# Performance work log

Measured on AMD Instinct MI355X. Metric: run time of the kernel, lower is better.

Reference implementation:

```python
import jax, jax.numpy as jnp
import numpy as np

E, H, I = 16, 2048, 768
B, S = 4, 1024
TOPK = 8
BLK_R, BLK_C = 128, 128


def blockwise_dequantize(w, scale_inv, r, c):
    # w: [E, M, N] (fp8 values stored as fp32 here), scale_inv: [E, M//r, N//c]
    e, m, n = w.shape
    wb = w.reshape(e, m // r, r, n // c, c)
    wb = wb * scale_inv[:, :, None, :, None]
    return wb.reshape(e, m, n)


def setup_inputs() -> dict:
    key = jax.random.key(0)
    ks = jax.random.split(key, 7)
    return {
        "hidden_states": jax.random.normal(ks[0], (B, S, H), dtype=jnp.float32),
        "routing_weights": jax.random.uniform(ks[1], (B * S, E), dtype=jnp.float32),
        "gate_up_proj": jax.random.normal(ks[2], (E, H, 2 * I), dtype=jnp.float32),
        "gate_up_proj_scale_inv": jax.random.uniform(ks[3], (E, H // BLK_R, 2 * I // BLK_C), dtype=jnp.float32),
        "down_proj": jax.random.normal(ks[4], (E, I, H), dtype=jnp.float32),
        "down_proj_scale_inv": jax.random.uniform(ks[5], (E, I // BLK_R, H // BLK_C), dtype=jnp.float32),
        "router_indices": jax.random.randint(ks[6], (B * S, TOPK), 0, E, dtype=jnp.int64 if jax.config.jax_enable_x64 else jnp.int32),
    }


def reference(hidden_states, routing_weights, gate_up_proj, gate_up_proj_scale_inv,
              down_proj, down_proj_scale_inv, router_indices):
    batch_size = hidden_states.shape[0]
    hs = hidden_states.reshape(-1, H)                      # [T, H], T = B*S
    x = jnp.broadcast_to(hs[None], (E,) + hs.shape)        # repeat across experts

    gu_w = blockwise_dequantize(gate_up_proj, gate_up_proj_scale_inv, BLK_R, BLK_C)   # [E, H, 2I]
    dn_w = blockwise_dequantize(down_proj, down_proj_scale_inv, BLK_R, BLK_C)         # [E, I, H]

    gate_up = jnp.einsum('eth,ehf->etf', x, gu_w)          # [E, T, 2I]
    gate, up = jnp.split(gate_up, 2, axis=-1)
    inter = up * jax.nn.silu(gate)                         # [E, T, I]
    next_states = jnp.einsum('eti,eih->eth', inter, dn_w)  # [E, T, H]

    next_states = next_states.reshape(E, batch_size, -1, H)
    rw = routing_weights.T.reshape(E, batch_size, -1)      # [E, B, S]
    out = (next_states * rw[..., None]).sum(axis=0)        # [B, S, H]
    return out
```

## Files before the change

kernel.cpp:

```cpp
#include <hip/hip_runtime.h>
#include <hip/hip_bf16.h>
#include <cstdint>

#define E_     16
#define H_     2048
#define I_     768
#define T_     4096
#define TWO_I  1536
#define K2_    (E_ * I_)
#define TILE_  (128 * 32)

typedef __bf16 bf16x8 __attribute__((ext_vector_type(8)));
typedef float  floatx4 __attribute__((ext_vector_type(4)));

__device__ __forceinline__ void gload_lds16(const void* g, void* l) {
  __builtin_amdgcn_global_load_lds(
      (const __attribute__((address_space(1))) void*)(void*)g,
      (__attribute__((address_space(3))) void*)l,
      16, 0, 0);
}

__global__ void k_convert(const float* __restrict__ in, __bf16* __restrict__ out) {
  size_t idx = ((size_t)blockIdx.x * blockDim.x + threadIdx.x) * 8;
  float4 a = *(const float4*)(in + idx);
  float4 b = *(const float4*)(in + idx + 4);
  bf16x8 o;
  o[0] = (__bf16)a.x; o[1] = (__bf16)a.y; o[2] = (__bf16)a.z; o[3] = (__bf16)a.w;
  o[4] = (__bf16)b.x; o[5] = (__bf16)b.y; o[6] = (__bf16)b.z; o[7] = (__bf16)b.w;
  *(bf16x8*)(out + idx) = o;
}

__global__ void k_dq_transpose(const float* __restrict__ src, __bf16* __restrict__ dst,
                               const float* __restrict__ scale, int R, int C,
                               size_t slab, size_t rowStride) {
  const int e  = blockIdx.z;
  const int n0 = blockIdx.x * 64;
  const int m0 = blockIdx.y * 64;
  __shared__ float tile[64 * 65];
  const float s = scale[((size_t)e * (R >> 7) + (m0 >> 7)) * (C >> 7) + (n0 >> 7)];
  const float* sp = src + ((size_t)e * R + m0) * C + n0;
  const int t  = threadIdx.x;
  const int c4 = (t & 15) * 4;
  const int rb = t >> 4;
  #pragma unroll
  for (int p = 0; p < 4; ++p) {
    int r = p * 16 + rb;
    float4 v = *(const float4*)(sp + (size_t)r * C + c4);
    tile[(c4 + 0) * 65 + r] = v.x * s;
    tile[(c4 + 1) * 65 + r] = v.y * s;
    tile[(c4 + 2) * 65 + r] = v.z * s;
    tile[(c4 + 3) * 65 + r] = v.w * s;
  }
  __syncthreads();
  __bf16* dp = dst + (size_t)e * slab + (size_t)n0 * rowStride + m0;
  const int c8 = (t & 7) * 8;
  const int r0 = t >> 3;
  #pragma unroll
  for (int p = 0; p < 2; ++p) {
    int nr = r0 + p * 32;
    const float* row = &tile[nr * 65 + c8];
    bf16x8 o;
    #pragma unroll
    for (int j = 0; j < 8; ++j) o[j] = (__bf16)row[j];
    *(bf16x8*)(dp + (size_t)nr * rowStride + c8) = o;
  }
}

__global__ __launch_bounds__(256, 2)
void k_gemm1(const __bf16* __restrict__ A, const __bf16* __restrict__ W,
             const float* __restrict__ rw, __bf16* __restrict__ inter) {
  const int e  = blockIdx.z;
  const int m0 = blockIdx.x * 128;
  const int i0 = blockIdx.y * 128;
  __shared__ __bf16 sA[2 * TILE_];
  __shared__ __bf16 sBg[2 * TILE_];
  __shared__ __bf16 sBu[2 * TILE_];
  __shared__ float sRW[128];
  const int t = threadIdx.x;
  const int wave = t >> 6, lane = t & 63;
  if (t < 128) sRW[t] = rw[(size_t)(m0 + t) * E_ + e];

  const int srow = lane >> 2;
  const int scol = (lane & 3) * 8;
  const int wm = wave >> 1, wn = wave & 1;
  const int r16 = lane & 15, kh = (lane >> 4) * 8;

  const size_t off0 = (size_t)(wave * 16 + srow) * H_ + scol;
  const size_t off1 = (size_t)((4 + wave) * 16 + srow) * H_ + scol;
  const __bf16* pa = A + (size_t)m0 * H_;
  const __bf16* pg = W + ((size_t)e * TWO_I + i0) * H_;
  const __bf16* pu = pg + (size_t)I_ * H_;
  __bf16* lA0 = &sA[(wave * 16) * 32];
  __bf16* lA1 = &sA[((4 + wave) * 16) * 32];
  __bf16* lG0 = &sBg[(wave * 16) * 32];
  __bf16* lG1 = &sBg[((4 + wave) * 16) * 32];
  __bf16* lU0 = &sBu[(wave * 16) * 32];
  __bf16* lU1 = &sBu[((4 + wave) * 16) * 32];

  floatx4 accg[4][4], accu[4][4];
  #pragma unroll
  for (int mi = 0; mi < 4; ++mi)
    #pragma unroll
    for (int ni = 0; ni < 4; ++ni) {
      floatx4 z = {0.f, 0.f, 0.f, 0.f};
      accg[mi][ni] = z; accu[mi][ni] = z;
    }

  for (int k0 = 0; k0 < H_; k0 += 64) {
    #pragma unroll
    for (int h = 0; h < 2; ++h) {
      const int kb = k0 + h * 32;
      const int ho = h * TILE_;
      gload_lds16(pa + off0 + kb, lA0 + ho);
      gload_lds16(pa + off1 + kb, lA1 + ho);
      gload_lds16(pg + off0 + kb, lG0 + ho);
      gload_lds16(pg + off1 + kb, lG1 + ho);
      gload_lds16(pu + off0 + kb, lU0 + ho);
      gload_lds16(pu + off1 + kb, lU1 + ho);
    }
    __syncthreads();
    #pragma unroll
    for (int h = 0; h < 2; ++h) {
      const int ho = h * TILE_;
      bf16x8 af[4], bg[4], bu[4];
      #pragma unroll
      for (int mi = 0; mi < 4; ++mi)
        af[mi] = *(const bf16x8*)&sA[ho + (wm * 64 + mi * 16 + r16) * 32 + kh];
      #pragma unroll
      for (int ni = 0; ni < 4; ++ni) {
        bg[ni] = *(const bf16x8*)&sBg[ho + (wn * 64 + ni * 16 + r16) * 32 + kh];
        bu[ni] = *(const bf16x8*)&sBu[ho + (wn * 64 + ni * 16 + r16) * 32 + kh];
      }
      #pragma unroll
      for (int mi = 0; mi < 4; ++mi)
        #pragma unroll
        for (int ni = 0; ni < 4; ++ni) {
          accg[mi][ni] = __builtin_amdgcn_mfma_f32_16x16x32_bf16(af[mi], bg[ni], accg[mi][ni], 0, 0, 0);
          accu[mi][ni] = __builtin_amdgcn_mfma_f32_16x16x32_bf16(af[mi], bu[ni], accu[mi][ni], 0, 0, 0);
        }
    }
    __syncthreads();
  }

  const int rq = (lane >> 4) * 4;
  #pragma unroll
  for (int mi = 0; mi < 4; ++mi) {
    #pragma unroll
    for (int ni = 0; ni < 4; ++ni) {
      const int cl = wn * 64 + ni * 16 + r16;
      #pragma unroll
      for (int r = 0; r < 4; ++r) {
        const int rl = wm * 64 + mi * 16 + rq + r;
        float g = accg[mi][ni][r];
        float u = accu[mi][ni][r];
        float sil = g / (1.0f + __expf(-g));
        float val = u * sil * sRW[rl];
        inter[(size_t)(m0 + rl) * K2_ + (size_t)e * I_ + i0 + cl] = (__bf16)val;
      }
    }
  }
}

__global__ __launch_bounds__(256, 2)
void k_gemm2(const __bf16* __restrict__ Ainter, const __bf16* __restrict__ W,
             float* __restrict__ out) {
  const int m0 = blockIdx.x * 128;
  const int n0 = blockIdx.y * 128;
  __shared__ __bf16 sA[2 * TILE_];
  __shared__ __bf16 sB[2 * TILE_];
  const int t = threadIdx.x;
  const int wave = t >> 6, lane = t & 63;
  const int srow = lane >> 2, scol = (lane & 3) * 8;
  const int wm = wave >> 1, wn = wave & 1;
  const int r16 = lane & 15, kh = (lane >> 4) * 8;

  const size_t off0 = (size_t)(wave * 16 + srow) * K2_ + scol;
  const size_t off1 = (size_t)((4 + wave) * 16 + srow) * K2_ + scol;
  const __bf16* pa = Ainter + (size_t)m0 * K2_;
  const __bf16* pb = W + (size_t)n0 * K2_;
  __bf16* lA0 = &sA[(wave * 16) * 32];
  __bf16* lA1 = &sA[((4 + wave) * 16) * 32];
  __bf16* lB0 = &sB[(wave * 16) * 32];
  __bf16* lB1 = &sB[((4 + wave) * 16) * 32];

  floatx4 acc[4][4];
  #pragma unroll
  for (int mi = 0; mi < 4; ++mi)
    #pragma unroll
    for (int ni = 0; ni < 4; ++ni) {
      floatx4 z = {0.f, 0.f, 0.f, 0.f};
      acc[mi][ni] = z;
    }

  for (int k0 = 0; k0 < K2_; k0 += 64) {
    #pragma unroll
    for (int h = 0; h < 2; ++h) {
      const int kb = k0 + h * 32;
      const int ho = h * TILE_;
      gload_lds16(pa + off0 + kb, lA0 + ho);
      gload_lds16(pa + off1 + kb, lA1 + ho);
      gload_lds16(pb + off0 + kb, lB0 + ho);
      gload_lds16(pb + off1 + kb, lB1 + ho);
    }
    __syncthreads();
    #pragma unroll
    for (int h = 0; h < 2; ++h) {
      const int ho = h * TILE_;
      bf16x8 af[4], bb[4];
      #pragma unroll
      for (int mi = 0; mi < 4; ++mi)
        af[mi] = *(const bf16x8*)&sA[ho + (wm * 64 + mi * 16 + r16) * 32 + kh];
      #pragma unroll
      for (int ni = 0; ni < 4; ++ni)
        bb[ni] = *(const bf16x8*)&sB[ho + (wn * 64 + ni * 16 + r16) * 32 + kh];
      #pragma unroll
      for (int mi = 0; mi < 4; ++mi)
        #pragma unroll
        for (int ni = 0; ni < 4; ++ni)
          acc[mi][ni] = __builtin_amdgcn_mfma_f32_16x16x32_bf16(af[mi], bb[ni], acc[mi][ni], 0, 0, 0);
    }
    __syncthreads();
  }

  const int rq = (lane >> 4) * 4;
  #pragma unroll
  for (int mi = 0; mi < 4; ++mi)
    #pragma unroll
    for (int ni = 0; ni < 4; ++ni) {
      const int cl = wn * 64 + ni * 16 + r16;
      #pragma unroll
      for (int r = 0; r < 4; ++r) {
        const int rl = wm * 64 + mi * 16 + rq + r;
        out[(size_t)(m0 + rl) * H_ + n0 + cl] = acc[mi][ni][r];
      }
    }
}

extern "C" void kernel_launch(void* const* d_in, const int* in_sizes, int n_in,
                              void* d_out, int out_size, void* d_ws, size_t ws_size,
                              hipStream_t stream) {
  const float* hs   = (const float*)d_in[0];
  const float* rw   = (const float*)d_in[1];
  const float* gup  = (const float*)d_in[2];
  const float* gups = (const float*)d_in[3];
  const float* dnp  = (const float*)d_in[4];
  const float* dnps = (const float*)d_in[5];
  float* out = (float*)d_out;

  char* ws = (char*)d_ws;
  __bf16* hsb  = (__bf16*)ws;
  __bf16* wgu  = (__bf16*)(ws + (size_t)(16 << 20));
  __bf16* wdn  = (__bf16*)(ws + (size_t)(112 << 20));
  __bf16* intr = (__bf16*)(ws + (size_t)(160 << 20));

  k_convert<<<(T_ * H_) / (256 * 8), 256, 0, stream>>>(hs, hsb);
  k_dq_transpose<<<dim3(TWO_I / 64, H_ / 64, E_), 256, 0, stream>>>(
      gup, wgu, gups, H_, TWO_I, (size_t)TWO_I * H_, (size_t)H_);
  k_dq_transpose<<<dim3(H_ / 64, I_ / 64, E_), 256, 0, stream>>>(
      dnp, wdn, dnps, I_, H_, (size_t)I_, (size_t)K2_);
  k_gemm1<<<dim3(T_ / 128, I_ / 128, E_), 256, 0, stream>>>(hsb, wgu, rw, intr);
  k_gemm2<<<dim3(T_ / 128, H_ / 128), 256, 0, stream>>>(intr, wdn, out);
}
```

Measured before the change: 1.078 ms.

## Rewrite MoE GEMMs with 256x256 tiles, swizzled LDS, pipelined staging and split-K

Both GEMMs move to 512-thread blocks computing 256x256 tiles, with XOR-swizzled LDS layouts and a double-buffered, phase-interleaved prefetch schedule built from explicit waitcnt, barriers and setprio. The gate and up weights are interleaved in 32-column groups by the dequant-transpose kernel, so a single B tile holds matching gate and up columns. The down projection is split over K into two halves that accumulate into a zeroed output with atomic adds. This aims to raise MFMA utilization and data reuse per LDS load, at the cost of about 128KB of dynamic LDS per block, atomic traffic and an extra memset.

```diff
diff --git a/kernel.cpp b/kernel.cpp
--- a/kernel.cpp
+++ b/kernel.cpp
@@ -8,7 +8,6 @@
 #define T_     4096
 #define TWO_I  1536
 #define K2_    (E_ * I_)
-#define TILE_  (128 * 32)
 
 typedef __bf16 bf16x8 __attribute__((ext_vector_type(8)));
 typedef float  floatx4 __attribute__((ext_vector_type(4)));
@@ -19,6 +18,11 @@
       (__attribute__((address_space(3))) void*)l,
       16, 0, 0);
 }
+
+#define ASM_VMCNT(n) asm volatile("s_waitcnt vmcnt(" #n ")" ::: "memory")
+#define ASM_LGKM0()  asm volatile("s_waitcnt lgkmcnt(0)" ::: "memory")
+#define SBAR()       __builtin_amdgcn_s_barrier()
+#define SCHED0()     __builtin_amdgcn_sched_barrier(0)
 
 __global__ void k_convert(const float* __restrict__ in, __bf16* __restrict__ out) {
   size_t idx = ((size_t)blockIdx.x * blockDim.x + threadIdx.x) * 8;
@@ -32,7 +36,7 @@
 
 __global__ void k_dq_transpose(const float* __restrict__ src, __bf16* __restrict__ dst,
                                const float* __restrict__ scale, int R, int C,
-                               size_t slab, size_t rowStride) {
+                               size_t slab, size_t rowStride, int ilvHalf) {
   const int e  = blockIdx.z;
   const int n0 = blockIdx.x * 64;
   const int m0 = blockIdx.y * 64;
@@ -52,188 +56,222 @@
     tile[(c4 + 3) * 65 + r] = v.w * s;
   }
   __syncthreads();
-  __bf16* dp = dst + (size_t)e * slab + (size_t)n0 * rowStride + m0;
   const int c8 = (t & 7) * 8;
   const int r0 = t >> 3;
   #pragma unroll
   for (int p = 0; p < 2; ++p) {
     int nr = r0 + p * 32;
+    int ng = n0 + nr;
+    int np;
+    if (ilvHalf) {
+      int h = (ng >= ilvHalf) ? 1 : 0;
+      int iLoc = ng - h * ilvHalf;
+      np = ((iLoc >> 5) << 6) + h * 32 + (iLoc & 31);
+    } else {
+      np = ng;
+    }
     const float* row = &tile[nr * 65 + c8];
     bf16x8 o;
     #pragma unroll
     for (int j = 0; j < 8; ++j) o[j] = (__bf16)row[j];
-    *(bf16x8*)(dp + (size_t)nr * rowStride + c8) = o;
-  }
-}
-
-__global__ __launch_bounds__(256, 2)
+    *(bf16x8*)(dst + (size_t)e * slab + (size_t)np * rowStride + m0 + c8) = o;
+  }
+}
+
+
+#define STG_A(tt, h) do { int b_ = ((tt)&1)*16384 + (h)*8192; \
+    gload_lds16(aSrc + (size_t)((h)*128)*LDK + (tt)*64, dA + b_); \
+    gload_lds16(aSrc + (size_t)((h)*128 + 64)*LDK + (tt)*64, dA + b_ + 4096); } while (0)
+#define STG_B(tt, h) do { int b_ = ((tt)&1)*16384 + (h)*8192; \
+    gload_lds16(bSrc + (size_t)((h)*128)*LDK + (tt)*64, dB + b_); \
+    gload_lds16(bSrc + (size_t)((h)*128 + 64)*LDK + (tt)*64, dB + b_ + 4096); } while (0)
+
+#define AF4(MI0) do { \
+    af[0][0] = *(const bf16x8*)(pA + (MI0)*1024 + kc0); \
+    af[0][1] = *(const bf16x8*)(pA + (MI0)*1024 + kc1); \
+    af[1][0] = *(const bf16x8*)(pA + ((MI0)+1)*1024 + kc0); \
+    af[1][1] = *(const bf16x8*)(pA + ((MI0)+1)*1024 + kc1); } while (0)
+
+#define MFMA16(MI0) do { \
+    _Pragma("unroll") \
+    for (int ii = 0; ii < 2; ++ii) { \
+      _Pragma("unroll") \
+      for (int ni = 0; ni < 4; ++ni) { \
+        acc[(MI0)+ii][ni] = __builtin_amdgcn_mfma_f32_16x16x32_bf16(af[ii][0], bb[ni][0], acc[(MI0)+ii][ni], 0, 0, 0); \
+        acc[(MI0)+ii][ni] = __builtin_amdgcn_mfma_f32_16x16x32_bf16(af[ii][1], bb[ni][1], acc[(MI0)+ii][ni], 0, 0, 0); \
+      } \
+    } } while (0)
+
+#define PHASE(MI0, STAGE_STMT, CKPT_STMT) do { \
+    AF4(MI0); \
+    STAGE_STMT; \
+    CKPT_STMT; \
+    SBAR(); \
+    ASM_LGKM0(); \
+    SCHED0(); \
+    __builtin_amdgcn_s_setprio(1); \
+    MFMA16(MI0); \
+    __builtin_amdgcn_s_setprio(0); \
+    SBAR(); \
+  } while (0)
+
+__global__ __launch_bounds__(512, 2)
 void k_gemm1(const __bf16* __restrict__ A, const __bf16* __restrict__ W,
              const float* __restrict__ rw, __bf16* __restrict__ inter) {
+  extern __shared__ __align__(16) __bf16 smem[];
+  __bf16* sA = smem;
+  __bf16* sB = smem + 32768;
+  float*  sRW = (float*)(smem + 65536);
+
   const int e  = blockIdx.z;
-  const int m0 = blockIdx.x * 128;
-  const int i0 = blockIdx.y * 128;
-  __shared__ __bf16 sA[2 * TILE_];
-  __shared__ __bf16 sBg[2 * TILE_];
-  __shared__ __bf16 sBu[2 * TILE_];
-  __shared__ float sRW[128];
-  const int t = threadIdx.x;
+  const int m0 = blockIdx.x * 256;
+  const int by = blockIdx.y;
+  const int n0 = by * 256;
+  const int t    = threadIdx.x;
   const int wave = t >> 6, lane = t & 63;
-  if (t < 128) sRW[t] = rw[(size_t)(m0 + t) * E_ + e];
-
-  const int srow = lane >> 2;
-  const int scol = (lane & 3) * 8;
-  const int wm = wave >> 1, wn = wave & 1;
-  const int r16 = lane & 15, kh = (lane >> 4) * 8;
-
-  const size_t off0 = (size_t)(wave * 16 + srow) * H_ + scol;
-  const size_t off1 = (size_t)((4 + wave) * 16 + srow) * H_ + scol;
-  const __bf16* pa = A + (size_t)m0 * H_;
-  const __bf16* pg = W + ((size_t)e * TWO_I + i0) * H_;
-  const __bf16* pu = pg + (size_t)I_ * H_;
-  __bf16* lA0 = &sA[(wave * 16) * 32];
-  __bf16* lA1 = &sA[((4 + wave) * 16) * 32];
-  __bf16* lG0 = &sBg[(wave * 16) * 32];
-  __bf16* lG1 = &sBg[((4 + wave) * 16) * 32];
-  __bf16* lU0 = &sBu[(wave * 16) * 32];
-  __bf16* lU1 = &sBu[((4 + wave) * 16) * 32];
-
-  floatx4 accg[4][4], accu[4][4];
-  #pragma unroll
-  for (int mi = 0; mi < 4; ++mi)
+  const int wm = wave >> 2, wn = wave & 3;
+  const int l4 = lane >> 4, r16 = lane & 15;
+  const int LDK = H_;
+
+  if (t < 256) sRW[t] = rw[(size_t)(m0 + t) * E_ + e];
+  ASM_VMCNT(0);
+
+  const int rowSt = t >> 3;
+  const int kcSt  = ((t & 7) ^ ((t >> 3) & 7)) << 3;
+  const __bf16* aSrc = A + (size_t)(m0 + rowSt) * H_ + kcSt;
+  const __bf16* bSrc = W + ((size_t)e * TWO_I + n0 + rowSt) * H_ + kcSt;
+  __bf16* dA = sA + wave * 512;
+  __bf16* dB = sB + wave * 512;
+
+  const int kc0 = (l4 ^ (r16 & 7)) << 3;
+  const int kc1 = ((4 + l4) ^ (r16 & 7)) << 3;
+  const __bf16* pArd = sA + wm * 8192 + r16 * 64;
+  const __bf16* pBrd = sB + (wn >> 1) * 8192 + ((wn & 1) * 64 + r16) * 64;
+
+  floatx4 acc[8][4];
+  #pragma unroll
+  for (int mi = 0; mi < 8; ++mi)
     #pragma unroll
     for (int ni = 0; ni < 4; ++ni) {
       floatx4 z = {0.f, 0.f, 0.f, 0.f};
-      accg[mi][ni] = z; accu[mi][ni] = z;
-    }
-
-  for (int k0 = 0; k0 < H_; k0 += 64) {
-    #pragma unroll
-    for (int h = 0; h < 2; ++h) {
-      const int kb = k0 + h * 32;
-      const int ho = h * TILE_;
-      gload_lds16(pa + off0 + kb, lA0 + ho);
-      gload_lds16(pa + off1 + kb, lA1 + ho);
-      gload_lds16(pg + off0 + kb, lG0 + ho);
-      gload_lds16(pg + off1 + kb, lG1 + ho);
-      gload_lds16(pu + off0 + kb, lU0 + ho);
-      gload_lds16(pu + off1 + kb, lU1 + ho);
-    }
-    __syncthreads();
-    #pragma unroll
-    for (int h = 0; h < 2; ++h) {
-      const int ho = h * TILE_;
-      bf16x8 af[4], bg[4], bu[4];
+      acc[mi][ni] = z;
+    }
+
+  STG_B(0, 0); STG_B(0, 1); STG_A(0, 0); STG_A(0, 1);
+  STG_B(1, 0); STG_B(1, 1);
+  ASM_VMCNT(4);
+  SBAR();
+
+  const int NT = H_ / 64;
+  for (int tt = 0; tt < NT; ++tt) {
+    const int bo = (tt & 1) * 16384;
+    const __bf16* pA = pArd + bo;
+    const __bf16* pB = pBrd + bo;
+    bf16x8 bb[4][2], af[2][2];
+    #pragma unroll
+    for (int ni = 0; ni < 4; ++ni) {
+      bb[ni][0] = *(const bf16x8*)(pB + ni * 1024 + kc0);
+      bb[ni][1] = *(const bf16x8*)(pB + ni * 1024 + kc1);
+    }
+    PHASE(0, if (tt + 1 < NT) STG_A(tt + 1, 0), (void)0);
+    PHASE(2, if (tt + 1 < NT) STG_A(tt + 1, 1), (void)0);
+    PHASE(4, if (tt + 2 < NT) STG_B(tt + 2, 0), (void)0);
+    PHASE(6, if (tt + 2 < NT) STG_B(tt + 2, 1),
+             if (tt + 2 < NT) { ASM_VMCNT(4); } else { ASM_VMCNT(0); });
+  }
+
+  const int rq = l4 * 4;
+  const int gBase = (by * 4 + wn) * 32;
+  #pragma unroll
+  for (int mi = 0; mi < 8; ++mi) {
+    const int rl = wm * 128 + mi * 16 + rq;
+    #pragma unroll
+    for (int ni = 0; ni < 2; ++ni) {
+      const size_t colIdx = (size_t)e * I_ + gBase + ni * 16 + r16;
       #pragma unroll
-      for (int mi = 0; mi < 4; ++mi)
-        af[mi] = *(const bf16x8*)&sA[ho + (wm * 64 + mi * 16 + r16) * 32 + kh];
-      #pragma unroll
-      for (int ni = 0; ni < 4; ++ni) {
-        bg[ni] = *(const bf16x8*)&sBg[ho + (wn * 64 + ni * 16 + r16) * 32 + kh];
-        bu[ni] = *(const bf16x8*)&sBu[ho + (wn * 64 + ni * 16 + r16) * 32 + kh];
+      for (int r = 0; r < 4; ++r) {
+        float g = acc[mi][ni][r];
+        float u = acc[mi][ni + 2][r];
+        float sil = g / (1.0f + __expf(-g));
+        float val = u * sil * sRW[rl + r];
+        inter[(size_t)(m0 + rl + r) * K2_ + colIdx] = (__bf16)val;
       }
-      #pragma unroll
-      for (int mi = 0; mi < 4; ++mi)
-        #pragma unroll
-        for (int ni = 0; ni < 4; ++ni) {
-          accg[mi][ni] = __builtin_amdgcn_mfma_f32_16x16x32_bf16(af[mi], bg[ni], accg[mi][ni], 0, 0, 0);
-          accu[mi][ni] = __builtin_amdgcn_mfma_f32_16x16x32_bf16(af[mi], bu[ni], accu[mi][ni], 0, 0, 0);
-        }
-    }
-    __syncthreads();
-  }
-
-  const int rq = (lane >> 4) * 4;
-  #pragma unroll
-  for (int mi = 0; mi < 4; ++mi) {
+    }
+  }
+}
+
+__global__ __launch_bounds__(512, 2)
+void k_gemm2(const __bf16* __restrict__ Ainter, const __bf16* __restrict__ W,
+             float* __restrict__ out) {
+  extern __shared__ __align__(16) __bf16 smem[];
+  __bf16* sA = smem;
+  __bf16* sB = smem + 32768;
+
+  const int m0 = blockIdx.x * 256;
+  const int n0 = blockIdx.y * 256;
+  const size_t kOff = (size_t)blockIdx.z * (K2_ / 2);
+  const int t    = threadIdx.x;
+  const int wave = t >> 6, lane = t & 63;
+  const int wm = wave >> 2, wn = wave & 3;
+  const int l4 = lane >> 4, r16 = lane & 15;
+  const int LDK = K2_;
+
+  const int rowSt = t >> 3;
+  const int kcSt  = ((t & 7) ^ ((t >> 3) & 7)) << 3;
+  const __bf16* aSrc = Ainter + (size_t)(m0 + rowSt) * K2_ + kOff + kcSt;
+  const __bf16* bSrc = W      + (size_t)(n0 + rowSt) * K2_ + kOff + kcSt;
+  __bf16* dA = sA + wave * 512;
+  __bf16* dB = sB + wave * 512;
+
+  const int kc0 = (l4 ^ (r16 & 7)) << 3;
+  const int kc1 = ((4 + l4) ^ (r16 & 7)) << 3;
+  const __bf16* pArd = sA + wm * 8192 + r16 * 64;
+  const __bf16* pBrd = sB + (wn >> 1) * 8192 + ((wn & 1) * 64 + r16) * 64;
+
+  floatx4 acc[8][4];
+  #pragma unroll
+  for (int mi = 0; mi < 8; ++mi)
+    #pragma unroll
+    for (int ni = 0; ni < 4; ++ni) {
+      floatx4 z = {0.f, 0.f, 0.f, 0.f};
+      acc[mi][ni] = z;
+    }
+
+  STG_B(0, 0); STG_B(0, 1); STG_A(0, 0); STG_A(0, 1);
+  STG_B(1, 0); STG_B(1, 1);
+  ASM_VMCNT(4);
+  SBAR();
+
+  const int NT = (K2_ / 2) / 64;
+  for (int tt = 0; tt < NT; ++tt) {
+    const int bo = (tt & 1) * 16384;
+    const __bf16* pA = pArd + bo;
+    const __bf16* pB = pBrd + bo;
+    bf16x8 bb[4][2], af[2][2];
+    #pragma unroll
+    for (int ni = 0; ni < 4; ++ni) {
+      bb[ni][0] = *(const bf16x8*)(pB + ni * 1024 + kc0);
+      bb[ni][1] = *(const bf16x8*)(pB + ni * 1024 + kc1);
+    }
+    PHASE(0, if (tt + 1 < NT) STG_A(tt + 1, 0), (void)0);
+    PHASE(2, if (tt + 1 < NT) STG_A(tt + 1, 1), (void)0);
+    PHASE(4, if (tt + 2 < NT) STG_B(tt + 2, 0), (void)0);
+    PHASE(6, if (tt + 2 < NT) STG_B(tt + 2, 1),
+             if (tt + 2 < NT) { ASM_VMCNT(4); } else { ASM_VMCNT(0); });
+  }
+
+  const int rq = l4 * 4;
+  #pragma unroll
+  for (int mi = 0; mi < 8; ++mi) {
+    const int rl = wm * 128 + mi * 16 + rq;
     #pragma unroll
     for (int ni = 0; ni < 4; ++ni) {
       const int cl = wn * 64 + ni * 16 + r16;
       #pragma unroll
-      for (int r = 0; r < 4; ++r) {
-        const int rl = wm * 64 + mi * 16 + rq + r;
-        float g = accg[mi][ni][r];
-        float u = accu[mi][ni][r];
-        float sil = g / (1.0f + __expf(-g));
-        float val = u * sil * sRW[rl];
-        inter[(size_t)(m0 + rl) * K2_ + (size_t)e * I_ + i0 + cl] = (__bf16)val;
-      }
-    }
-  }
-}
-
-__global__ __launch_bounds__(256, 2)
-void k_gemm2(const __bf16* __restrict__ Ainter, const __bf16* __restrict__ W,
-             float* __restrict__ out) {
-  const int m0 = blockIdx.x * 128;
-  const int n0 = blockIdx.y * 128;
-  __shared__ __bf16 sA[2 * TILE_];
-  __shared__ __bf16 sB[2 * TILE_];
-  const int t = threadIdx.x;
-  const int wave = t >> 6, lane = t & 63;
-  const int srow = lane >> 2, scol = (lane & 3) * 8;
-  const int wm = wave >> 1, wn = wave & 1;
-  const int r16 = lane & 15, kh = (lane >> 4) * 8;
-
-  const size_t off0 = (size_t)(wave * 16 + srow) * K2_ + scol;
-  const size_t off1 = (size_t)((4 + wave) * 16 + srow) * K2_ + scol;
-  const __bf16* pa = Ainter + (size_t)m0 * K2_;
-  const __bf16* pb = W + (size_t)n0 * K2_;
-  __bf16* lA0 = &sA[(wave * 16) * 32];
-  __bf16* lA1 = &sA[((4 + wave) * 16) * 32];
-  __bf16* lB0 = &sB[(wave * 16) * 32];
-  __bf16* lB1 = &sB[((4 + wave) * 16) * 32];
-
-  floatx4 acc[4][4];
-  #pragma unroll
-  for (int mi = 0; mi < 4; ++mi)
-    #pragma unroll
-    for (int ni = 0; ni < 4; ++ni) {
-      floatx4 z = {0.f, 0.f, 0.f, 0.f};
-      acc[mi][ni] = z;
-    }
-
-  for (int k0 = 0; k0 < K2_; k0 += 64) {
-    #pragma unroll
-    for (int h = 0; h < 2; ++h) {
-      const int kb = k0 + h * 32;
-      const int ho = h * TILE_;
-      gload_lds16(pa + off0 + kb, lA0 + ho);
-      gload_lds16(pa + off1 + kb, lA1 + ho);
-      gload_lds16(pb + off0 + kb, lB0 + ho);
-      gload_lds16(pb + off1 + kb, lB1 + ho);
-    }
-    __syncthreads();
-    #pragma unroll
-    for (int h = 0; h < 2; ++h) {
-      const int ho = h * TILE_;
-      bf16x8 af[4], bb[4];
-      #pragma unroll
-      for (int mi = 0; mi < 4; ++mi)
-        af[mi] = *(const bf16x8*)&sA[ho + (wm * 64 + mi * 16 + r16) * 32 + kh];
-      #pragma unroll
-      for (int ni = 0; ni < 4; ++ni)
-        bb[ni] = *(const bf16x8*)&sB[ho + (wn * 64 + ni * 16 + r16) * 32 + kh];
-      #pragma unroll
-      for (int mi = 0; mi < 4; ++mi)
-        #pragma unroll
-        for (int ni = 0; ni < 4; ++ni)
-          acc[mi][ni] = __builtin_amdgcn_mfma_f32_16x16x32_bf16(af[mi], bb[ni], acc[mi][ni], 0, 0, 0);
-    }
-    __syncthreads();
-  }
-
-  const int rq = (lane >> 4) * 4;
-  #pragma unroll
-  for (int mi = 0; mi < 4; ++mi)
-    #pragma unroll
-    for (int ni = 0; ni < 4; ++ni) {
-      const int cl = wn * 64 + ni * 16 + r16;
-      #pragma unroll
-      for (int r = 0; r < 4; ++r) {
-        const int rl = wm * 64 + mi * 16 + rq + r;
-        out[(size_t)(m0 + rl) * H_ + n0 + cl] = acc[mi][ni][r];
-      }
-    }
+      for (int r = 0; r < 4; ++r)
+        unsafeAtomicAdd(out + (size_t)(m0 + rl + r) * H_ + n0 + cl, acc[mi][ni][r]);
+    }
+  }
 }
 
 extern "C" void kernel_launch(void* const* d_in, const int* in_sizes, int n_in,
@@ -253,11 +291,22 @@
   __bf16* wdn  = (__bf16*)(ws + (size_t)(112 << 20));
   __bf16* intr = (__bf16*)(ws + (size_t)(160 << 20));
 
+  static int inited = 0;
+  if (!inited) {
+    hipFuncSetAttribute((const void*)k_gemm1,
+                        hipFuncAttributeMaxDynamicSharedMemorySize, 132096);
+    hipFuncSetAttribute((const void*)k_gemm2,
+                        hipFuncAttributeMaxDynamicSharedMemorySize, 131072);
+    inited = 1;
+  }
+
+  hipMemsetAsync(out, 0, (size_t)T_ * H_ * sizeof(float), stream);
+
   k_convert<<<(T_ * H_) / (256 * 8), 256, 0, stream>>>(hs, hsb);
   k_dq_transpose<<<dim3(TWO_I / 64, H_ / 64, E_), 256, 0, stream>>>(
-      gup, wgu, gups, H_, TWO_I, (size_t)TWO_I * H_, (size_t)H_);
+      gup, wgu, gups, H_, TWO_I, (size_t)TWO_I * H_, (size_t)H_, I_);
   k_dq_transpose<<<dim3(H_ / 64, I_ / 64, E_), 256, 0, stream>>>(
-      dnp, wdn, dnps, I_, H_, (size_t)I_, (size_t)K2_);
-  k_gemm1<<<dim3(T_ / 128, I_ / 128, E_), 256, 0, stream>>>(hsb, wgu, rw, intr);
-  k_gemm2<<<dim3(T_ / 128, H_ / 128), 256, 0, stream>>>(intr, wdn, out);
-}
+      dnp, wdn, dnps, I_, H_, (size_t)I_, (size_t)K2_, 0);
+  k_gemm1<<<dim3(T_ / 256, TWO_I / 256, E_), 512, 132096, stream>>>(hsb, wgu, rw, intr);
+  k_gemm2<<<dim3(T_ / 256, H_ / 256, 2), 512, 131072, stream>>>(intr, wdn, out);
+}
```

Result: faster. 927.6 us (-14.0%).
